# Kernel optimization log

Measured on AMD Instinct MI355X. Metric: run time of the kernel, lower is better.

Reference implementation:

```python
import jax, jax.numpy as jnp
import numpy as np

B, S, DM, H = 2, 2048, 1024, 16        # dim_model = d_model//2 = 1024
WINDOW, DILATION, N_GLOBAL = 513, 2, 32
HD = DM // H
NEG = -1e9


def build_mask(n, window_size, dilation, global_idx):
    # dilated local window: |i-j| <= (window//2)*dilation and (i-j) % dilation == 0
    i = jnp.arange(n)[:, None]
    j = jnp.arange(n)[None, :]
    d = j - i
    half = window_size // 2
    local = (jnp.abs(d) <= half * dilation) & (jnp.mod(d, dilation) == 0)
    g = jnp.zeros((n,), bool).at[global_idx].set(True)
    # symmetric global token mask: global rows and columns fully attend
    return local | g[:, None] | g[None, :]


def setup_inputs() -> dict:
    key = jax.random.key(0)
    ks = jax.random.split(key, 9)
    std = 0.02
    inp = {
        "q": jax.random.normal(ks[0], (B, S, DM), jnp.float32),
        "k": jax.random.normal(ks[1], (B, S, DM), jnp.float32),
        "v": jax.random.normal(ks[2], (B, S, DM), jnp.float32),
        "Wq": jax.random.normal(ks[3], (DM, DM), jnp.float32) * std,
        "Wk": jax.random.normal(ks[4], (DM, DM), jnp.float32) * std,
        "Wv": jax.random.normal(ks[5], (DM, DM), jnp.float32) * std,
        "Wo": jax.random.normal(ks[6], (DM, DM), jnp.float32) * std,
        "bq": jnp.zeros((DM,), jnp.float32),
        "bk": jnp.zeros((DM,), jnp.float32),
        "bv": jnp.zeros((DM,), jnp.float32),
        "bo": jnp.zeros((DM,), jnp.float32),
        "global_idx": jax.random.randint(ks[7], (N_GLOBAL,), 0, S, jnp.int64)
        if jax.config.jax_enable_x64 else jax.random.randint(ks[7], (N_GLOBAL,), 0, S, jnp.int32),
    }
    return inp


def reference(q, k, v, Wq, Wk, Wv, Wo, bq, bk, bv, bo, global_idx):
    def split(x):  # [B,S,DM] -> [B,H,S,HD]
        return x.reshape(B, S, H, HD).transpose(0, 2, 1, 3)

    qh = split(q @ Wq.T + bq)
    kh = split(k @ Wk.T + bk)
    vh = split(v @ Wv.T + bv)

    scores = jnp.einsum("bhqd,bhkd->bhqk", qh, kh) / jnp.sqrt(jnp.asarray(HD, qh.dtype))
    mask = build_mask(S, WINDOW, DILATION, global_idx)  # [S,S] bool
    scores = jnp.where(mask[None, None], scores, NEG)
    attn = jax.nn.softmax(scores, axis=-1)
    out = jnp.einsum("bhqk,bhkd->bhqd", attn, vh)
    out = out.transpose(0, 2, 1, 3).reshape(B, S, DM)
    return out @ Wo.T + bo
```

## Files before the change

### kernel.cpp

```cpp
#include <hip/hip_runtime.h>
#include <hip/hip_bf16.h>
#include <math.h>

#define BB 2
#define SS 2048
#define DMM 1024
#define HH 16
#define HDD 64
#define NGLOB 32
#define MM 4096
#define SCALE2 0.18033688f

typedef __attribute__((ext_vector_type(8))) short short8;
typedef __attribute__((ext_vector_type(4))) float float4v;

__device__ __forceinline__ short f2bf(float f) {
    union { float f; unsigned u; } x; x.f = f;
    unsigned r = (x.u + 0x7fffu + ((x.u >> 16) & 1u)) >> 16;
    return (short)r;
}

#define ASYNC16(gp, lp) __builtin_amdgcn_global_load_lds( \
    (__attribute__((address_space(1))) void*)(gp), \
    (__attribute__((address_space(3))) void*)(lp), 16, 0, 0)

#define VSL(dim, key) ((dim) * 40 + (((((key) >> 3) ^ (((dim) >> 3) & 3)) << 3) | ((key) & 7)))

__global__ void setup_globals(const int* __restrict__ gidx, int* __restrict__ g,
                              int* __restrict__ glist, int* __restrict__ gcount) {
    int t = threadIdx.x;
    for (int i = t; i < SS; i += 256) g[i] = 0;
    if (t == 0) *gcount = 0;
    __syncthreads();
    if (t < NGLOB) {
        int j = gidx[t];
        if (j >= 0 && j < SS) g[j] = 1;
    }
    __syncthreads();
    for (int j = t; j < SS; j += 256) {
        if (g[j]) {
            int p = atomicAdd(gcount, 1);
            glist[p] = j;
        }
    }
}

__global__ __launch_bounds__(256)
void convert_all(const float* __restrict__ q, const float* __restrict__ k,
                 const float* __restrict__ v,
                 const float* __restrict__ w0, const float* __restrict__ w1,
                 const float* __restrict__ w2, const float* __restrict__ w3,
                 short* __restrict__ abf, short* __restrict__ wbf) {
    int z = blockIdx.y;
    const float* src;
    short* dst;
    size_t n;
    if (z < 3) {
        src = (z == 0) ? q : (z == 1) ? k : v;
        dst = abf + (size_t)z * ((size_t)MM * DMM);
        n = (size_t)MM * DMM;
    } else {
        int y = z - 3;
        src = (y == 0) ? w0 : (y == 1) ? w1 : (y == 2) ? w2 : w3;
        dst = wbf + (size_t)y * ((size_t)DMM * DMM);
        n = (size_t)DMM * DMM;
    }
    size_t i = ((size_t)blockIdx.x * 256 + threadIdx.x) * 8;
    if (i >= n) return;
    float4 a = *(const float4*)(src + i);
    float4 b = *(const float4*)(src + i + 4);
    short8 s;
    s[0]=f2bf(a.x); s[1]=f2bf(a.y); s[2]=f2bf(a.z); s[3]=f2bf(a.w);
    s[4]=f2bf(b.x); s[5]=f2bf(b.y); s[6]=f2bf(b.z); s[7]=f2bf(b.w);
    *(short8*)(dst + i) = s;
}

template<int OBF, int HEADSPLIT>
__global__ __launch_bounds__(256)
void gemm128(const short* __restrict__ Abase, const short* __restrict__ Wbase,
             const float* __restrict__ b0, const float* __restrict__ b1,
             const float* __restrict__ b2,
             void* __restrict__ O0p, void* __restrict__ O1p, void* __restrict__ O2p) {
    __shared__ short As[3][128 * 32];
    __shared__ short Ws[3][128 * 32];

    int t = threadIdx.x;
    int z = blockIdx.y;
    const short* A    = Abase + (size_t)z * ((size_t)MM * DMM);
    const short* W    = Wbase + (size_t)z * ((size_t)DMM * DMM);
    const float* bias = (z == 0) ? b0 : (z == 1) ? b1 : b2;
    void* outp        = (z == 0) ? O0p : (z == 1) ? O1p : O2p;

    int bid = blockIdx.x;
    int xcd = bid & 7, loc = bid >> 3;
    int nblk = loc & 7, mloc = loc >> 3;
    int m0 = (xcd * 4 + mloc) * 128;
    int n0 = nblk * 128;

    int lane = t & 63, w = t >> 6;
    int quad = lane >> 4, col = lane & 15;
    int wr = (w & 1) * 64;
    int wc = (w >> 1) * 64;

    float4v acc[4][4];
    #pragma unroll
    for (int i = 0; i < 4; i++)
        #pragma unroll
        for (int j = 0; j < 4; j++) acc[i][j] = (float4v){0, 0, 0, 0};

    int rowA = t >> 2,  kcA = (t & 3) * 8;
    const short* Ap = A + (size_t)(m0 + rowA) * DMM + kcA;
    const short* Wp = W + (size_t)(n0 + rowA) * DMM + kcA;

    #define STAGE(bf, tt) do { int kk = (tt) * 32; \
        ASYNC16(Ap + kk,                      &As[bf][t * 8]); \
        ASYNC16(Ap + 64 * (size_t)DMM + kk,   &As[bf][2048 + t * 8]); \
        ASYNC16(Wp + kk,                      &Ws[bf][t * 8]); \
        ASYNC16(Wp + 64 * (size_t)DMM + kk,   &Ws[bf][2048 + t * 8]); \
    } while (0)

    STAGE(0, 0);
    STAGE(1, 1);

    int cur = 0;
    for (int it = 0; it < 32; it++) {
        if (it < 31) asm volatile("s_waitcnt vmcnt(4)" ::: "memory");
        else         asm volatile("s_waitcnt vmcnt(0)" ::: "memory");
        __builtin_amdgcn_s_barrier();

        int sb = cur - 1; if (sb < 0) sb = 2;
        if (it + 2 < 32) STAGE(sb, it + 2);

        short8 aF[4], bF[4];
        #pragma unroll
        for (int i = 0; i < 4; i++)
            aF[i] = *(short8*)&As[cur][(wr + 16 * i + col) * 32 + quad * 8];
        #pragma unroll
        for (int j = 0; j < 4; j++)
            bF[j] = *(short8*)&Ws[cur][(wc + 16 * j + col) * 32 + quad * 8];

        #pragma unroll
        for (int i = 0; i < 4; i++)
            #pragma unroll
            for (int j = 0; j < 4; j++)
                acc[i][j] = __builtin_amdgcn_mfma_f32_16x16x32_bf16(aF[i], bF[j], acc[i][j], 0, 0, 0);

        cur++; if (cur == 3) cur = 0;
    }
    #undef STAGE

    #pragma unroll
    for (int i = 0; i < 4; i++) {
        #pragma unroll
        for (int j = 0; j < 4; j++) {
            int n = n0 + wc + 16 * j + col;
            float bn = bias[n];
            #pragma unroll
            for (int r = 0; r < 4; r++) {
                int m = m0 + wr + 16 * i + quad * 4 + r;
                float val = acc[i][j][r] + bn;
                size_t idx;
                if (HEADSPLIT) {
                    int b = m >> 11;
                    int s = m & 2047;
                    int h = n >> 6;
                    int hd = n & 63;
                    idx = (((size_t)b * HH + h) * SS + s) * HDD + hd;
                } else {
                    idx = (size_t)m * DMM + n;
                }
                if (OBF) ((short*)outp)[idx] = f2bf(val);
                else     ((float*)outp)[idx] = val;
            }
        }
    }
}

__global__ __launch_bounds__(256)
void band_attn(const short* __restrict__ qh, const short* __restrict__ kh,
               const short* __restrict__ vh, const int* __restrict__ glist,
               const int* __restrict__ gcount, short* __restrict__ ao) {
    __shared__ short Qs[64 * 72];
    __shared__ short Ks[32 * 72];
    __shared__ short Vt[64 * 40];
    __shared__ short Ps[4 * 16 * 40];
    __shared__ int   gjs[32];

    int t = threadIdx.x;
    int bid = blockIdx.x;
    int xcd = bid & 7, idx = bid >> 3;
    int gl  = idx >> 4;
    int qt  = idx & 15;
    int gid = xcd * 8 + gl;
    int z   = gid >> 4;
    int h   = gid & 15;
    int b = z >> 1, p = z & 1;
    int qq0 = qt * 64;
    int nG = *gcount;

    const short* Qb = qh + ((size_t)(b * HH + h) * SS) * HDD;
    const short* Kb = kh + ((size_t)(b * HH + h) * SS) * HDD;
    const short* Vb = vh + ((size_t)(b * HH + h) * SS) * HDD;

    int row8 = t >> 3;
    int dim8 = (t & 7) * 8;

    #pragma unroll
    for (int rr = 0; rr < 2; rr++) {
        int row = rr * 32 + row8;
        int i = 2 * (qq0 + row) + p;
        short8 qv = *(const short8*)(Qb + (size_t)i * HDD + dim8);
        *(short8*)&Qs[row * 72 + dim8] = qv;
    }
    if (t < 32) gjs[t] = (t < nG) ? glist[t] : -1000000;
    __syncthreads();

    int lane = t & 63, w = t >> 6;
    int quad = lane >> 4, col = lane & 15;

    short8 qf0 = *(short8*)&Qs[(16 * w + col) * 72 + quad * 8];
    short8 qf1 = *(short8*)&Qs[(16 * w + col) * 72 + 32 + quad * 8];

    float4v O0 = {0,0,0,0}, O1 = {0,0,0,0}, O2 = {0,0,0,0}, O3 = {0,0,0,0};
    float lst[4] = {0.f, 0.f, 0.f, 0.f};

    for (int c = 0; c < 19; c++) {
        __syncthreads();
        int ch0 = qq0 - 256 + c * 32;
        int srow;
        if (c < 18) srow = 2 * (ch0 + row8) + p;
        else        srow = (row8 < nG) ? gjs[row8] : 0;
        srow = srow < 0 ? 0 : (srow > SS - 1 ? SS - 1 : srow);
        short8 kv = *(const short8*)(Kb + (size_t)srow * HDD + dim8);
        short8 vv = *(const short8*)(Vb + (size_t)srow * HDD + dim8);
        *(short8*)&Ks[row8 * 72 + dim8] = kv;
        #pragma unroll
        for (int j = 0; j < 8; j++) {
            int d = dim8 + j;
            Vt[VSL(d, row8)] = vv[j];
        }
        __syncthreads();

        short8 kA0 = *(short8*)&Ks[col * 72 + quad * 8];
        short8 kA1 = *(short8*)&Ks[col * 72 + 32 + quad * 8];
        short8 kB0 = *(short8*)&Ks[(16 + col) * 72 + quad * 8];
        short8 kB1 = *(short8*)&Ks[(16 + col) * 72 + 32 + quad * 8];
        float4v sA = {0,0,0,0}, sB = {0,0,0,0};
        sA = __builtin_amdgcn_mfma_f32_16x16x32_bf16(qf0, kA0, sA, 0, 0, 0);
        sA = __builtin_amdgcn_mfma_f32_16x16x32_bf16(qf1, kA1, sA, 0, 0, 0);
        sB = __builtin_amdgcn_mfma_f32_16x16x32_bf16(qf0, kB0, sB, 0, 0, 0);
        sB = __builtin_amdgcn_mfma_f32_16x16x32_bf16(qf1, kB1, sB, 0, 0, 0);

        if (c < 18) {
            int nlo = -ch0;
            int nhi = 1023 - ch0;
            #pragma unroll
            for (int r = 0; r < 4; r++) {
                int qq = qq0 + 16 * w + quad * 4 + r;
                int u  = qq - ch0;
                int lo = max(u - 256, nlo);
                int hi = min(u + 256, nhi);
                bool vA = (col >= lo) && (col <= hi);
                bool vB = (col + 16 >= lo) && (col + 16 <= hi);
                float pa = vA ? exp2f(sA[r] * SCALE2) : 0.f;
                float pb = vB ? exp2f(sB[r] * SCALE2) : 0.f;
                lst[r] += pa + pb;
                Ps[(w * 16 + quad * 4 + r) * 40 + col]      = f2bf(pa);
                Ps[(w * 16 + quad * 4 + r) * 40 + col + 16] = f2bf(pb);
            }
        } else {
            #pragma unroll
            for (int r = 0; r < 4; r++) {
                int qq = qq0 + 16 * w + quad * 4 + r;
                int i = 2 * qq + p;
                int jA = gjs[col], jB = gjs[col + 16];
                int dA = jA - i, dB = jB - i;
                int aA = dA < 0 ? -dA : dA;
                int aB = dB < 0 ? -dB : dB;
                bool vA = (jA >= 0) && !((aA <= 512) && ((dA & 1) == 0));
                bool vB = (jB >= 0) && !((aB <= 512) && ((dB & 1) == 0));
                float pa = vA ? exp2f(sA[r] * SCALE2) : 0.f;
                float pb = vB ? exp2f(sB[r] * SCALE2) : 0.f;
                lst[r] += pa + pb;
                Ps[(w * 16 + quad * 4 + r) * 40 + col]      = f2bf(pa);
                Ps[(w * 16 + quad * 4 + r) * 40 + col + 16] = f2bf(pb);
            }
        }
        asm volatile("s_waitcnt lgkmcnt(0)" ::: "memory");

        short8 pf  = *(short8*)&Ps[(w * 16 + col) * 40 + quad * 8];
        short8 vf0 = *(short8*)&Vt[(col) * 40 + ((quad ^ ((col >> 3) & 3)) << 3)];
        short8 vf1 = *(short8*)&Vt[(16 + col) * 40 + ((quad ^ (((16 + col) >> 3) & 3)) << 3)];
        short8 vf2 = *(short8*)&Vt[(32 + col) * 40 + ((quad ^ (((32 + col) >> 3) & 3)) << 3)];
        short8 vf3 = *(short8*)&Vt[(48 + col) * 40 + ((quad ^ (((48 + col) >> 3) & 3)) << 3)];
        O0 = __builtin_amdgcn_mfma_f32_16x16x32_bf16(pf, vf0, O0, 0, 0, 0);
        O1 = __builtin_amdgcn_mfma_f32_16x16x32_bf16(pf, vf1, O1, 0, 0, 0);
        O2 = __builtin_amdgcn_mfma_f32_16x16x32_bf16(pf, vf2, O2, 0, 0, 0);
        O3 = __builtin_amdgcn_mfma_f32_16x16x32_bf16(pf, vf3, O3, 0, 0, 0);
    }

    #pragma unroll
    for (int r = 0; r < 4; r++) {
        float l = lst[r];
        #pragma unroll
        for (int mk = 1; mk < 16; mk <<= 1) l += __shfl_xor(l, mk);
        float inv = 1.0f / l;
        int q = 16 * w + quad * 4 + r;
        int i = 2 * (qq0 + q) + p;
        short* dst = ao + ((size_t)b * SS + i) * DMM + h * HDD;
        dst[col]      = f2bf(O0[r] * inv);
        dst[col + 16] = f2bf(O1[r] * inv);
        dst[col + 32] = f2bf(O2[r] * inv);
        dst[col + 48] = f2bf(O3[r] * inv);
    }
}

__global__ __launch_bounds__(256)
void global_part(const short* __restrict__ qh, const short* __restrict__ kh,
                 const short* __restrict__ vh, const int* __restrict__ glist,
                 const int* __restrict__ gcount,
                 float* __restrict__ pl, float* __restrict__ pO) {
    __shared__ short Qs[32 * 72];
    __shared__ short Ks[2][32 * 72];
    __shared__ short Vt[2][64 * 40];
    __shared__ short Ps[4 * 16 * 40];

    int t = threadIdx.x;
    int s = blockIdx.x, h = blockIdx.y, b = blockIdx.z;
    int nG = *gcount;

    const short* Qb = qh + ((size_t)(b * HH + h) * SS) * HDD;
    const short* Kb = kh + ((size_t)(b * HH + h) * SS) * HDD;
    const short* Vb = vh + ((size_t)(b * HH + h) * SS) * HDD;

    int row8 = t >> 3, dim8 = (t & 7) * 8;
    {
        int cq = row8 < nG ? row8 : 0;
        int src = glist[cq];
        short8 qv = *(const short8*)(Qb + (size_t)src * HDD + dim8);
        *(short8*)&Qs[row8 * 72 + dim8] = qv;
    }
    __syncthreads();

    int lane = t & 63, w = t >> 6;
    int quad = lane >> 4, col = lane & 15;
    int g = w >> 1, qt = w & 1;

    short8 qf0 = *(short8*)&Qs[(qt * 16 + col) * 72 + quad * 8];
    short8 qf1 = *(short8*)&Qs[(qt * 16 + col) * 72 + 32 + quad * 8];

    float4v O0 = {0,0,0,0}, O1 = {0,0,0,0}, O2 = {0,0,0,0}, O3 = {0,0,0,0};
    float lst[4] = {0.f, 0.f, 0.f, 0.f};

    int js0 = s * 256;
    for (int it = 0; it < 4; it++) {
        __syncthreads();
        int r64 = t >> 2, dimb = (t & 3) * 16;
        int j = js0 + it * 64 + r64;
        const short* kp = Kb + (size_t)j * HDD + dimb;
        const short* vp = Vb + (size_t)j * HDD + dimb;
        short8 k0 = *(const short8*)kp, k1 = *(const short8*)(kp + 8);
        short8 v0 = *(const short8*)vp, v1 = *(const short8*)(vp + 8);
        int half = r64 >> 5, r32 = r64 & 31;
        *(short8*)&Ks[half][r32 * 72 + dimb]     = k0;
        *(short8*)&Ks[half][r32 * 72 + dimb + 8] = k1;
        #pragma unroll
        for (int u = 0; u < 8; u++) {
            int d = dimb + u;
            Vt[half][VSL(d, r32)] = v0[u];
        }
        #pragma unroll
        for (int u = 0; u < 8; u++) {
            int d = dimb + 8 + u;
            Vt[half][VSL(d, r32)] = v1[u];
        }
        __syncthreads();

        short8 kA0 = *(short8*)&Ks[g][col * 72 + quad * 8];
        short8 kA1 = *(short8*)&Ks[g][col * 72 + 32 + quad * 8];
        short8 kB0 = *(short8*)&Ks[g][(16 + col) * 72 + quad * 8];
        short8 kB1 = *(short8*)&Ks[g][(16 + col) * 72 + 32 + quad * 8];
        float4v sA = {0,0,0,0}, sB = {0,0,0,0};
        sA = __builtin_amdgcn_mfma_f32_16x16x32_bf16(qf0, kA0, sA, 0, 0, 0);
        sA = __builtin_amdgcn_mfma_f32_16x16x32_bf16(qf1, kA1, sA, 0, 0, 0);
        sB = __builtin_amdgcn_mfma_f32_16x16x32_bf16(qf0, kB0, sB, 0, 0, 0);
        sB = __builtin_amdgcn_mfma_f32_16x16x32_bf16(qf1, kB1, sB, 0, 0, 0);

        #pragma unroll
        for (int r = 0; r < 4; r++) {
            float pa = exp2f(sA[r] * SCALE2);
            float pb = exp2f(sB[r] * SCALE2);
            lst[r] += pa + pb;
            Ps[(w * 16 + quad * 4 + r) * 40 + col]      = f2bf(pa);
            Ps[(w * 16 + quad * 4 + r) * 40 + col + 16] = f2bf(pb);
        }
        asm volatile("s_waitcnt lgkmcnt(0)" ::: "memory");

        short8 pf  = *(short8*)&Ps[(w * 16 + col) * 40 + quad * 8];
        short8 vf0 = *(short8*)&Vt[g][(col) * 40 + ((quad ^ ((col >> 3) & 3)) << 3)];
        short8 vf1 = *(short8*)&Vt[g][(16 + col) * 40 + ((quad ^ (((16 + col) >> 3) & 3)) << 3)];
        short8 vf2 = *(short8*)&Vt[g][(32 + col) * 40 + ((quad ^ (((32 + col) >> 3) & 3)) << 3)];
        short8 vf3 = *(short8*)&Vt[g][(48 + col) * 40 + ((quad ^ (((48 + col) >> 3) & 3)) << 3)];
        O0 = __builtin_amdgcn_mfma_f32_16x16x32_bf16(pf, vf0, O0, 0, 0, 0);
        O1 = __builtin_amdgcn_mfma_f32_16x16x32_bf16(pf, vf1, O1, 0, 0, 0);
        O2 = __builtin_amdgcn_mfma_f32_16x16x32_bf16(pf, vf2, O2, 0, 0, 0);
        O3 = __builtin_amdgcn_mfma_f32_16x16x32_bf16(pf, vf3, O3, 0, 0, 0);
    }

    int sp = s * 2 + g;
    size_t base = ((size_t)(b * HH + h) * 16 + sp) * 32;
    #pragma unroll
    for (int r = 0; r < 4; r++) {
        float l = lst[r];
        #pragma unroll
        for (int mk = 1; mk < 16; mk <<= 1) l += __shfl_xor(l, mk);
        int q = qt * 16 + quad * 4 + r;
        if (col == 0) pl[base + q] = l;
        float* Od = pO + (base + q) * 64;
        Od[col]      = O0[r];
        Od[col + 16] = O1[r];
        Od[col + 32] = O2[r];
        Od[col + 48] = O3[r];
    }
}

__global__ __launch_bounds__(256)
void global_merge(const float* __restrict__ pl, const float* __restrict__ pO,
                  const int* __restrict__ glist, const int* __restrict__ gcount,
                  short* __restrict__ ao) {
    int h = blockIdx.x, b = blockIdx.y;
    int t = threadIdx.x;
    int d = t & 63, qg = t >> 6;
    int nG = *gcount;
    size_t bh = ((size_t)(b * HH + h) * 16) * 32;

    for (int q = qg; q < nG; q += 4) {
        float L = 0.f, acc = 0.f;
        #pragma unroll
        for (int sp = 0; sp < 16; sp++) {
            L   += pl[bh + sp * 32 + q];
            acc += pO[(bh + sp * 32 + q) * 64 + d];
        }
        int i = glist[q];
        ao[((size_t)b * SS + i) * DMM + h * HDD + d] = f2bf(acc / L);
    }
}

extern "C" void kernel_launch(void* const* d_in, const int* in_sizes, int n_in,
                              void* d_out, int out_size, void* d_ws, size_t ws_size,
                              hipStream_t stream) {
    const float* q  = (const float*)d_in[0];
    const float* k  = (const float*)d_in[1];
    const float* v  = (const float*)d_in[2];
    const float* Wq = (const float*)d_in[3];
    const float* Wk = (const float*)d_in[4];
    const float* Wv = (const float*)d_in[5];
    const float* Wo = (const float*)d_in[6];
    const float* bq = (const float*)d_in[7];
    const float* bk = (const float*)d_in[8];
    const float* bv = (const float*)d_in[9];
    const float* bo = (const float*)d_in[10];
    const int* gidx = (const int*)d_in[11];
    float* out = (float*)d_out;

    const size_t NE = (size_t)BB * SS * DMM;
    const size_t WE = (size_t)DMM * DMM;
    int*   g      = (int*)d_ws;
    int*   glist  = g + SS;
    int*   gcount = glist + SS;
    short* qh     = (short*)((char*)d_ws + 32768);
    short* kh     = qh + NE;
    short* vh     = kh + NE;
    short* ao     = vh + NE;
    short* wbf    = ao + NE;
    short* wo     = wbf + 3 * WE;
    short* abf    = wbf + 4 * WE;
    float* pl     = (float*)abf;
    float* pO     = pl + 16384;

    setup_globals<<<1, 256, 0, stream>>>(gidx, g, glist, gcount);

    dim3 gc(2048, 7);
    convert_all<<<gc, 256, 0, stream>>>(q, k, v, Wq, Wk, Wv, Wo, abf, wbf);

    dim3 gq(256, 3);
    gemm128<1, 1><<<gq, 256, 0, stream>>>(abf, wbf, bq, bk, bv, qh, kh, vh);

    band_attn<<<1024, 256, 0, stream>>>(qh, kh, vh, glist, gcount, ao);

    dim3 gp(8, HH, BB);
    global_part<<<gp, 256, 0, stream>>>(qh, kh, vh, glist, gcount, pl, pO);

    dim3 gm(HH, BB);
    global_merge<<<gm, 256, 0, stream>>>(pl, pO, glist, gcount, ao);

    dim3 go(256, 1);
    gemm128<0, 0><<<go, 256, 0, stream>>>(ao, wo, bo, bo, bo, out, out, out);
}
```

Measured before the change: 236.3 us.

## Switch GEMM to double-buffered LDS and register-prefetch K/V chunks in attention

The projection GEMM drops from a triple-buffered async pipeline to double buffering, with a full vmcnt(0) wait and barrier after each k-step, and raises wave priority around the MFMA block with s_setprio. The attention kernel now loads the next K/V chunk into registers while the current chunk is stored to LDS and computed, so global-load latency is hidden behind MFMA work. The GEMM change cuts LDS use, which may allow higher occupancy, but it shortens the prefetch distance and adds a full memory wait every iteration. The attention prefetch uses more registers per thread.

```diff
diff --git a/kernel.cpp b/kernel.cpp
--- a/kernel.cpp
+++ b/kernel.cpp
@@ -81,8 +81,8 @@
              const float* __restrict__ b0, const float* __restrict__ b1,
              const float* __restrict__ b2,
              void* __restrict__ O0p, void* __restrict__ O1p, void* __restrict__ O2p) {
-    __shared__ short As[3][128 * 32];
-    __shared__ short Ws[3][128 * 32];
+    __shared__ short As[2][128 * 32];
+    __shared__ short Ws[2][128 * 32];
 
     int t = threadIdx.x;
     int z = blockIdx.y;
@@ -120,16 +120,12 @@
     } while (0)
 
     STAGE(0, 0);
-    STAGE(1, 1);
-
-    int cur = 0;
+    asm volatile("s_waitcnt vmcnt(0)" ::: "memory");
+    __builtin_amdgcn_s_barrier();
+
     for (int it = 0; it < 32; it++) {
-        if (it < 31) asm volatile("s_waitcnt vmcnt(4)" ::: "memory");
-        else         asm volatile("s_waitcnt vmcnt(0)" ::: "memory");
-        __builtin_amdgcn_s_barrier();
-
-        int sb = cur - 1; if (sb < 0) sb = 2;
-        if (it + 2 < 32) STAGE(sb, it + 2);
+        int cur = it & 1;
+        if (it + 1 < 32) STAGE(cur ^ 1, it + 1);
 
         short8 aF[4], bF[4];
         #pragma unroll
@@ -139,13 +135,16 @@
         for (int j = 0; j < 4; j++)
             bF[j] = *(short8*)&Ws[cur][(wc + 16 * j + col) * 32 + quad * 8];
 
+        __builtin_amdgcn_s_setprio(1);
         #pragma unroll
         for (int i = 0; i < 4; i++)
             #pragma unroll
             for (int j = 0; j < 4; j++)
                 acc[i][j] = __builtin_amdgcn_mfma_f32_16x16x32_bf16(aF[i], bF[j], acc[i][j], 0, 0, 0);
-
-        cur++; if (cur == 3) cur = 0;
+        __builtin_amdgcn_s_setprio(0);
+
+        asm volatile("s_waitcnt vmcnt(0)" ::: "memory");
+        __builtin_amdgcn_s_barrier();
     }
     #undef STAGE
 
@@ -224,22 +223,35 @@
     float4v O0 = {0,0,0,0}, O1 = {0,0,0,0}, O2 = {0,0,0,0}, O3 = {0,0,0,0};
     float lst[4] = {0.f, 0.f, 0.f, 0.f};
 
+    short8 kvP, vvP, kvN, vvN;
+    {
+        int srow = 2 * (qq0 - 256 + row8) + p;
+        srow = srow < 0 ? 0 : (srow > SS - 1 ? SS - 1 : srow);
+        kvP = *(const short8*)(Kb + (size_t)srow * HDD + dim8);
+        vvP = *(const short8*)(Vb + (size_t)srow * HDD + dim8);
+    }
+
     for (int c = 0; c < 19; c++) {
         __syncthreads();
-        int ch0 = qq0 - 256 + c * 32;
-        int srow;
-        if (c < 18) srow = 2 * (ch0 + row8) + p;
-        else        srow = (row8 < nG) ? gjs[row8] : 0;
-        srow = srow < 0 ? 0 : (srow > SS - 1 ? SS - 1 : srow);
-        short8 kv = *(const short8*)(Kb + (size_t)srow * HDD + dim8);
-        short8 vv = *(const short8*)(Vb + (size_t)srow * HDD + dim8);
-        *(short8*)&Ks[row8 * 72 + dim8] = kv;
+        *(short8*)&Ks[row8 * 72 + dim8] = kvP;
         #pragma unroll
         for (int j = 0; j < 8; j++) {
             int d = dim8 + j;
-            Vt[VSL(d, row8)] = vv[j];
+            Vt[VSL(d, row8)] = vvP[j];
+        }
+        if (c < 18) {
+            int cn = c + 1;
+            int ch0n = qq0 - 256 + cn * 32;
+            int srow;
+            if (cn < 18) srow = 2 * (ch0n + row8) + p;
+            else         srow = (row8 < nG) ? gjs[row8] : 0;
+            srow = srow < 0 ? 0 : (srow > SS - 1 ? SS - 1 : srow);
+            kvN = *(const short8*)(Kb + (size_t)srow * HDD + dim8);
+            vvN = *(const short8*)(Vb + (size_t)srow * HDD + dim8);
         }
         __syncthreads();
+
+        int ch0 = qq0 - 256 + c * 32;
 
         short8 kA0 = *(short8*)&Ks[col * 72 + quad * 8];
         short8 kA1 = *(short8*)&Ks[col * 72 + 32 + quad * 8];
@@ -297,6 +309,8 @@
         O1 = __builtin_amdgcn_mfma_f32_16x16x32_bf16(pf, vf1, O1, 0, 0, 0);
         O2 = __builtin_amdgcn_mfma_f32_16x16x32_bf16(pf, vf2, O2, 0, 0, 0);
         O3 = __builtin_amdgcn_mfma_f32_16x16x32_bf16(pf, vf3, O3, 0, 0, 0);
+
+        kvP = kvN; vvP = vvN;
     }
 
     #pragma unroll
```

Measured after the change: 234.8 us. No clear change (-0.6%).
